# Kernel tuning notes

Hardware: AMD Instinct MI355X
Metric: run time of the kernel (lower is better)

The kernel has to match this reference:

```python
import jax, jax.numpy as jnp
import numpy as np

VOCAB = 50000
EMBED = 256
BATCH = 16384
NUM_SAMPLED = 4096


def _log_uniform_prob(ids):
    # P(c) = (log(c+2) - log(c+1)) / log(V+1), the log-uniform sampler distribution
    ids = ids.astype(jnp.float32)
    return (jnp.log(ids + 2.0) - jnp.log(ids + 1.0)) / jnp.log(VOCAB + 1.0)


def _expected_count(ids, num_sampled):
    # unique log-uniform sampler expected count: 1 - (1 - p)^num_tries, num_tries ~= num_sampled
    p = _log_uniform_prob(ids)
    return -jnp.expm1(num_sampled * jnp.log1p(-p))


def _sigmoid_xent(logits, labels):
    # stable sigmoid cross-entropy: max(x,0) - x*z + log(1 + exp(-|x|))
    return jnp.maximum(logits, 0.0) - logits * labels + jnp.log1p(jnp.exp(-jnp.abs(logits)))


def setup_inputs() -> dict:
    key = jax.random.key(0)
    k1, k2, k3, k4 = jax.random.split(key, 4)
    embedding = jax.random.normal(k1, (BATCH, EMBED), dtype=jnp.float32)
    target_words = jax.random.randint(k2, (BATCH, 1), 0, VOCAB, dtype=jnp.int64 if jax.config.jax_enable_x64 else jnp.int32)
    sampled_ids = jax.random.randint(k3, (NUM_SAMPLED,), 0, VOCAB, dtype=jnp.int64 if jax.config.jax_enable_x64 else jnp.int32)
    # truncated-normal init with stddev 1/sqrt(embed_size), matching TruncatedNormal
    nce_weight = (jax.random.truncated_normal(k4, -2.0, 2.0, (VOCAB, EMBED), dtype=jnp.float32)
                  * (1.0 / EMBED ** 0.5))
    nce_bias = jnp.zeros((VOCAB,), dtype=jnp.float32)
    return {"embedding": embedding, "target_words": target_words,
            "sampled_ids": sampled_ids, "nce_weight": nce_weight, "nce_bias": nce_bias}


def reference(embedding, target_words, sampled_ids, nce_weight, nce_bias):
    num_sampled = sampled_ids.shape[0]
    labels = target_words[:, 0]                       # [B]

    # gather true-class rows and compute true logits (subtract_log_q=True in tf.nn.nce_loss)
    w_true = nce_weight[labels]                       # [B, D]
    true_logits = (jnp.sum(embedding * w_true, axis=-1) + nce_bias[labels]
                   - jnp.log(_expected_count(labels, num_sampled)))          # [B]

    # gather sampled rows and compute sampled logits
    w_samp = nce_weight[sampled_ids]                  # [S, D]
    sampled_logits = (jnp.einsum('bd,sd->bs', embedding, w_samp) + nce_bias[sampled_ids]
                      - jnp.log(_expected_count(sampled_ids, num_sampled)))  # [B, S]

    # sigmoid cross-entropy: true label 1, sampled labels 0; sum per example, mean over batch
    per_example = _sigmoid_xent(true_logits, 1.0) + jnp.sum(_sigmoid_xent(sampled_logits, 0.0), axis=-1)
    return jnp.mean(per_example)
```

## Files before the change

kernel.cpp:

```cpp
#include <hip/hip_runtime.h>
#include <cstdint>
#include <cstddef>

#define VOCAB 50000
#define EMBED 256
#define BATCH 16384
#define NSAMP 4096

typedef float f32x4 __attribute__((ext_vector_type(4)));
typedef int   i32x8 __attribute__((ext_vector_type(8)));


__device__ __forceinline__ f32x4 vsplat(float a) {
    f32x4 r = {a, a, a, a};
    return r;
}

__device__ __forceinline__ float log_expected_count(int id) {
    float u = 1.0f / ((float)id + 1.0f);
    float a = __logf(1.0f + u);
    float p = a * 0.09242324f;
    float ser = p * (1.0f + p * (0.5f + p * (0.33333333f + p * (0.25f + p * 0.2f))));
    float q = -(float)NSAMP * ser;
    return __logf(1.0f - __expf(q));
}

__device__ __forceinline__ float softplus_f(float x) {
    float v = __expf(-fabsf(x));
    float p = fmaf(v, 0.03215845f, -0.13606275f);
    p = fmaf(v, p, 0.28947478f);
    p = fmaf(v, p, -0.49190896f);
    p = fmaf(v, p, 0.99949556f);
    return fmaxf(x, 0.0f) + v * p;
}

__device__ __forceinline__ void softplus4_acc(f32x4 x, f32x4& vsum) {
    f32x4 ax = __builtin_elementwise_abs(x);
    f32x4 v;
    v.x = __expf(-ax.x);
    v.y = __expf(-ax.y);
    v.z = __expf(-ax.z);
    v.w = __expf(-ax.w);
    f32x4 p = __builtin_elementwise_fma(v, vsplat(0.03215845f), vsplat(-0.13606275f));
    p = __builtin_elementwise_fma(v, p, vsplat(0.28947478f));
    p = __builtin_elementwise_fma(v, p, vsplat(-0.49190896f));
    p = __builtin_elementwise_fma(v, p, vsplat(0.99949556f));
    vsum += __builtin_elementwise_max(x, vsplat(0.0f));
    vsum = __builtin_elementwise_fma(v, p, vsum);
}

__device__ __forceinline__ int pk4_fp8(float a, float b, float c, float d) {
    int v = __builtin_amdgcn_cvt_pk_fp8_f32(a, b, 0, false);
    v = __builtin_amdgcn_cvt_pk_fp8_f32(c, d, v, true);
    return v;
}



__global__ __launch_bounds__(256) void k_prep(
        const float* __restrict__ E, const int* __restrict__ tgt,
        const int* __restrict__ sids, const float* __restrict__ W,
        const float* __restrict__ bias,
        unsigned char* __restrict__ EF, unsigned char* __restrict__ BF,
        float* __restrict__ badj, double* __restrict__ pTrue)
{
    const int blk = blockIdx.x, tid = threadIdx.x;
    const int wave = tid >> 6, lane = tid & 63;

    if (blk < 1024) {
        float tsum = 0.0f;
        #pragma unroll
        for (int i = 0; i < 4; ++i) {
            int b = (blk * 4 + wave) + 4096 * i;
            int label = tgt[b];
            float4 e  = ((const float4*)(E + (size_t)b * EMBED))[lane];
            float4 wv = ((const float4*)(W + (size_t)label * EMBED))[lane];
            int pk = pk4_fp8(e.x, e.y, e.z, e.w);
            *(int*)(EF + ((b >> 4) * 4096 + (lane >> 3) * 512
                          + (b & 15) * 32 + (lane & 7) * 4)) = pk;
            float d = e.x * wv.x + e.y * wv.y + e.z * wv.z + e.w * wv.w;
            #pragma unroll
            for (int off = 32; off > 0; off >>= 1) d += __shfl_down(d, off, 64);
            if (lane == 0) {
                float tl = d + bias[label] - log_expected_count(label);
                tsum += softplus_f(-tl);
            }
        }
        __shared__ float ts[4];
        if (lane == 0) ts[wave] = tsum;
        __syncthreads();
        if (tid == 0) pTrue[blk] = (double)((ts[0] + ts[1]) + (ts[2] + ts[3]));
    } else {
        #pragma unroll
        for (int i = 0; i < 4; ++i) {
            int task = (blk - 1024) * 256 + tid + 16384 * i;
            int s = task >> 4, p = task & 15;
            int sid = sids[s];
            const float4* wr = (const float4*)(W + (size_t)sid * EMBED + p * 16);
            float4 w0 = wr[0], w1 = wr[1], w2 = wr[2], w3 = wr[3];
            int4 o;
            o.x = pk4_fp8(w0.x * 16.0f, w0.y * 16.0f, w0.z * 16.0f, w0.w * 16.0f);
            o.y = pk4_fp8(w1.x * 16.0f, w1.y * 16.0f, w1.z * 16.0f, w1.w * 16.0f);
            o.z = pk4_fp8(w2.x * 16.0f, w2.y * 16.0f, w2.z * 16.0f, w2.w * 16.0f);
            o.w = pk4_fp8(w3.x * 16.0f, w3.y * 16.0f, w3.z * 16.0f, w3.w * 16.0f);
            *(int4*)(BF + ((s >> 4) * 4096 + (p >> 1) * 512
                           + (s & 15) * 32 + (p & 1) * 16)) = o;
            if (p == 0) badj[s] = bias[sid] - log_expected_count(sid);
        }
    }
}

__global__ __launch_bounds__(256, 2) void k_gemm(
        const unsigned char* __restrict__ EF,
        const unsigned char* __restrict__ BF,
        const float* __restrict__ badj,
        double* __restrict__ pGemm)
{
    const int tid  = threadIdx.x;
    const int wave = tid >> 6;
    const int lane = tid & 63;
    const int rg   = blockIdx.x >> 4;
    const int cg   = blockIdx.x & 15;
    const int ag0  = rg * 16 + wave * 4;
    const int r16  = lane & 15;

    __shared__ unsigned char Blds[65536];

    i32x8 af[2][4];
    #pragma unroll
    for (int s = 0; s < 2; ++s)
        #pragma unroll
        for (int mi = 0; mi < 4; ++mi)
            af[s][mi] = *(const i32x8*)(EF + (size_t)(ag0 + mi) * 4096
                                        + s * 2048 + lane * 32);

    {
        const unsigned char* Bsrc = BF + (size_t)cg * 65536;
        #pragma unroll
        for (int it = 0; it < 16; ++it) {
            int woff = it * 4096 + wave * 1024;
            int goff = woff + lane * 16;
            __builtin_amdgcn_global_load_lds(
                (const __attribute__((address_space(1))) void*)(Bsrc + goff),
                (__attribute__((address_space(3))) void*)(Blds + woff),
                16, 0, 0);
        }
    }

    asm volatile("s_waitcnt vmcnt(0)");
    __syncthreads();

    #pragma unroll
    for (int s = 0; s < 2; ++s)
        #pragma unroll
        for (int mi = 0; mi < 4; ++mi)
            asm volatile("" : "+v"(af[s][mi]));

    f32x4 vsum = {};

    #pragma unroll 1
    for (int j = 0; j < 4; ++j) {
        i32x8 bf[2][4];
        #pragma unroll
        for (int s = 0; s < 2; ++s)
            #pragma unroll
            for (int ni = 0; ni < 4; ++ni)
                bf[s][ni] = *(const i32x8*)(Blds + (j * 4 + ni) * 4096
                                            + s * 2048 + lane * 32);

        float ba[4];
        #pragma unroll
        for (int ni = 0; ni < 4; ++ni)
            ba[ni] = badj[cg * 256 + j * 64 + ni * 16 + r16];

        #pragma unroll
        for (int mi = 0; mi < 4; ++mi) {
            f32x4 acc[4] = {};
            #pragma unroll
            for (int s = 0; s < 2; ++s)
                #pragma unroll
                for (int ni = 0; ni < 4; ++ni)
                    acc[ni] = __builtin_amdgcn_mfma_scale_f32_16x16x128_f8f6f4(
                        af[s][mi], bf[s][ni], acc[ni],
                        0, 0,
                        0, 0x7F7F7F7F,
                        0, 0x7B7B7B7B);
            #pragma unroll
            for (int ni = 0; ni < 4; ++ni)
                softplus4_acc(acc[ni] + ba[ni], vsum);
        }
    }

    float lsum = (vsum.x + vsum.y) + (vsum.z + vsum.w);
    #pragma unroll
    for (int off = 32; off > 0; off >>= 1) lsum += __shfl_down(lsum, off, 64);
    __shared__ float wsum[4];
    if (lane == 0) wsum[wave] = lsum;
    __syncthreads();
    if (tid == 0)
        pGemm[blockIdx.x] = (double)((wsum[0] + wsum[1]) + (wsum[2] + wsum[3]));
}

__global__ __launch_bounds__(256) void k_final(
        const double* __restrict__ pTrue, const double* __restrict__ pGemm,
        float* __restrict__ out)
{
    const int tid = threadIdx.x, wave = tid >> 6, lane = tid & 63;
    double s = 0.0;
    for (int i = tid; i < 1024; i += 256) s += pTrue[i];
    for (int i = tid; i < 1024; i += 256) s += pGemm[i];
    #pragma unroll
    for (int off = 32; off > 0; off >>= 1) s += __shfl_down(s, off, 64);
    __shared__ double wsum[4];
    if (lane == 0) wsum[wave] = s;
    __syncthreads();
    if (tid == 0)
        out[0] = (float)(((wsum[0] + wsum[1]) + (wsum[2] + wsum[3]))
                         * (1.0 / (double)BATCH));
}


extern "C" void kernel_launch(void* const* d_in, const int* in_sizes, int n_in,
                              void* d_out, int out_size, void* d_ws, size_t ws_size,
                              hipStream_t stream) {
    const float* emb  = (const float*)d_in[0];
    const int*   tgt  = (const int*)d_in[1];
    const int*   sids = (const int*)d_in[2];
    const float* W    = (const float*)d_in[3];
    const float* bias = (const float*)d_in[4];
    float* out = (float*)d_out;

    char* ws = (char*)d_ws;
    double*        pTrue = (double*)ws;
    double*        pGemm = (double*)(ws + 8192);
    float*         badj  = (float*)(ws + 40960);
    unsigned char* BF    = (unsigned char*)(ws + 57344);
    unsigned char* EF    = (unsigned char*)(ws + 57344 + 1048576);

    hipLaunchKernelGGL(k_prep, dim3(1088), dim3(256), 0, stream,
                       emb, tgt, sids, W, bias, EF, BF, badj, pTrue);
    hipLaunchKernelGGL(k_gemm, dim3(1024), dim3(256), 0, stream,
                       EF, BF, badj, pGemm);
    hipLaunchKernelGGL(k_final, dim3(1), dim3(256), 0, stream,
                       pTrue, pGemm, out);
}
```

Measured before the change: 130.6 us.

## Use 8-wave GEMM blocks with split-half B layout for conflict-free LDS reads

The GEMM block grows from 4 to 8 waves, each owning 2 instead of 4 A row-groups, to cut per-wave register use and raise the number of resident waves. The fp8 B tile is re-laid out so each lane reads two 16-byte chunks 256 bytes apart instead of one contiguous 32-byte chunk, aiming to reduce LDS bank conflicts. The loop is restructured so B fragments load per k-slice and feed 8 accumulators. The trade-off is more waves contending for LDS and more B reads per useful MFMA, since each B fragment is now reused across only 2 A tiles.

New measurement: 129.0 us. About the same (-1.2%).

```diff
diff --git a/kernel.cpp b/kernel.cpp
--- a/kernel.cpp
+++ b/kernel.cpp
@@ -8,6 +8,7 @@
 #define NSAMP 4096
 
 typedef float f32x4 __attribute__((ext_vector_type(4)));
+typedef int   i32x4 __attribute__((ext_vector_type(4)));
 typedef int   i32x8 __attribute__((ext_vector_type(8)));
 
 
@@ -103,14 +104,14 @@
             o.y = pk4_fp8(w1.x * 16.0f, w1.y * 16.0f, w1.z * 16.0f, w1.w * 16.0f);
             o.z = pk4_fp8(w2.x * 16.0f, w2.y * 16.0f, w2.z * 16.0f, w2.w * 16.0f);
             o.w = pk4_fp8(w3.x * 16.0f, w3.y * 16.0f, w3.z * 16.0f, w3.w * 16.0f);
-            *(int4*)(BF + ((s >> 4) * 4096 + (p >> 1) * 512
-                           + (s & 15) * 32 + (p & 1) * 16)) = o;
+            *(int4*)(BF + ((s >> 4) * 4096 + (p >> 1) * 512 + (p & 1) * 256
+                           + (s & 15) * 16)) = o;
             if (p == 0) badj[s] = bias[sid] - log_expected_count(sid);
         }
     }
 }
 
-__global__ __launch_bounds__(256, 2) void k_gemm(
+__global__ __launch_bounds__(512, 4) void k_gemm(
         const unsigned char* __restrict__ EF,
         const unsigned char* __restrict__ BF,
         const float* __restrict__ badj,
@@ -121,24 +122,25 @@
     const int lane = tid & 63;
     const int rg   = blockIdx.x >> 4;
     const int cg   = blockIdx.x & 15;
-    const int ag0  = rg * 16 + wave * 4;
+    const int ag0  = rg * 16 + wave * 2;
     const int r16  = lane & 15;
 
     __shared__ unsigned char Blds[65536];
-
-    i32x8 af[2][4];
+    __shared__ float wsum[8];
+
+    i32x8 af[2][2];
     #pragma unroll
     for (int s = 0; s < 2; ++s)
         #pragma unroll
-        for (int mi = 0; mi < 4; ++mi)
+        for (int mi = 0; mi < 2; ++mi)
             af[s][mi] = *(const i32x8*)(EF + (size_t)(ag0 + mi) * 4096
                                         + s * 2048 + lane * 32);
 
     {
         const unsigned char* Bsrc = BF + (size_t)cg * 65536;
         #pragma unroll
-        for (int it = 0; it < 16; ++it) {
-            int woff = it * 4096 + wave * 1024;
+        for (int it = 0; it < 8; ++it) {
+            int woff = it * 8192 + wave * 1024;
             int goff = woff + lane * 16;
             __builtin_amdgcn_global_load_lds(
                 (const __attribute__((address_space(1))) void*)(Bsrc + goff),
@@ -153,52 +155,60 @@
     #pragma unroll
     for (int s = 0; s < 2; ++s)
         #pragma unroll
-        for (int mi = 0; mi < 4; ++mi)
+        for (int mi = 0; mi < 2; ++mi)
             asm volatile("" : "+v"(af[s][mi]));
 
     f32x4 vsum = {};
+    const int lbase = (lane >> 4) * 512 + r16 * 16;
 
     #pragma unroll 1
     for (int j = 0; j < 4; ++j) {
-        i32x8 bf[2][4];
-        #pragma unroll
-        for (int s = 0; s < 2; ++s)
-            #pragma unroll
-            for (int ni = 0; ni < 4; ++ni)
-                bf[s][ni] = *(const i32x8*)(Blds + (j * 4 + ni) * 4096
-                                            + s * 2048 + lane * 32);
-
         float ba[4];
         #pragma unroll
         for (int ni = 0; ni < 4; ++ni)
             ba[ni] = badj[cg * 256 + j * 64 + ni * 16 + r16];
 
-        #pragma unroll
-        for (int mi = 0; mi < 4; ++mi) {
-            f32x4 acc[4] = {};
-            #pragma unroll
-            for (int s = 0; s < 2; ++s)
+        f32x4 acc[2][4] = {};
+        #pragma unroll
+        for (int s = 0; s < 2; ++s) {
+            i32x8 bf[4];
+            #pragma unroll
+            for (int ni = 0; ni < 4; ++ni) {
+                const unsigned char* bp = Blds + (j * 4 + ni) * 4096
+                                          + s * 2048 + lbase;
+                i32x4 lo = *(const i32x4*)bp;
+                i32x4 hi = *(const i32x4*)(bp + 256);
+                bf[ni][0] = lo[0]; bf[ni][1] = lo[1];
+                bf[ni][2] = lo[2]; bf[ni][3] = lo[3];
+                bf[ni][4] = hi[0]; bf[ni][5] = hi[1];
+                bf[ni][6] = hi[2]; bf[ni][7] = hi[3];
+            }
+            #pragma unroll
+            for (int mi = 0; mi < 2; ++mi)
                 #pragma unroll
                 for (int ni = 0; ni < 4; ++ni)
-                    acc[ni] = __builtin_amdgcn_mfma_scale_f32_16x16x128_f8f6f4(
-                        af[s][mi], bf[s][ni], acc[ni],
+                    acc[mi][ni] = __builtin_amdgcn_mfma_scale_f32_16x16x128_f8f6f4(
+                        af[s][mi], bf[ni], acc[mi][ni],
                         0, 0,
                         0, 0x7F7F7F7F,
                         0, 0x7B7B7B7B);
+        }
+
+        #pragma unroll
+        for (int mi = 0; mi < 2; ++mi)
             #pragma unroll
             for (int ni = 0; ni < 4; ++ni)
-                softplus4_acc(acc[ni] + ba[ni], vsum);
-        }
+                softplus4_acc(acc[mi][ni] + ba[ni], vsum);
     }
 
     float lsum = (vsum.x + vsum.y) + (vsum.z + vsum.w);
     #pragma unroll
     for (int off = 32; off > 0; off >>= 1) lsum += __shfl_down(lsum, off, 64);
-    __shared__ float wsum[4];
     if (lane == 0) wsum[wave] = lsum;
     __syncthreads();
     if (tid == 0)
-        pGemm[blockIdx.x] = (double)((wsum[0] + wsum[1]) + (wsum[2] + wsum[3]));
+        pGemm[blockIdx.x] = (double)((((wsum[0] + wsum[1]) + (wsum[2] + wsum[3]))
+                                    + ((wsum[4] + wsum[5]) + (wsum[6] + wsum[7]))));
 }
 
 __global__ __launch_bounds__(256) void k_final(
@@ -239,7 +249,7 @@
 
     hipLaunchKernelGGL(k_prep, dim3(1088), dim3(256), 0, stream,
                        emb, tgt, sids, W, bias, EF, BF, badj, pTrue);
-    hipLaunchKernelGGL(k_gemm, dim3(1024), dim3(256), 0, stream,
+    hipLaunchKernelGGL(k_gemm, dim3(1024), dim3(512), 0, stream,
                        EF, BF, badj, pGemm);
     hipLaunchKernelGGL(k_final, dim3(1), dim3(256), 0, stream,
                        pTrue, pGemm, out);
```
